# Optimization experiments

Measured on AMD Instinct MI355X. Metric: run time of the kernel, lower is better.

The kernel has to match this reference:

```python
import jax, jax.numpy as jnp
import numpy as np

N = 100000      # nodes
D_IN = 512      # in_size
D_OUT = 512     # out_size
E = 200000      # edges per etype
EPS = 1e-5      # LayerNorm eps


def setup_inputs() -> dict:
    key = jax.random.key(0)
    ks = jax.random.split(key, 10)
    scale = 1.0 / np.sqrt(D_IN)
    inp = {
        "x": jax.random.normal(ks[0], (N, D_IN), jnp.float32),
        "W0": jax.random.normal(ks[1], (D_OUT, D_IN), jnp.float32) * scale,
        "W1": jax.random.normal(ks[2], (D_OUT, D_IN), jnp.float32) * scale,
        "W2": jax.random.normal(ks[3], (D_OUT, D_IN), jnp.float32) * scale,
        "gamma": jnp.ones((D_OUT,), jnp.float32),
        "beta": jnp.zeros((D_OUT,), jnp.float32),
        "src0": jax.random.randint(ks[4], (E,), 0, N, jnp.int32),
        "dst0": jax.random.randint(ks[5], (E,), 0, N, jnp.int32),
        "src1": jax.random.randint(ks[6], (E,), 0, N, jnp.int32),
        "dst1": jax.random.randint(ks[7], (E,), 0, N, jnp.int32),
        "src2": jax.random.randint(ks[8], (E,), 0, N, jnp.int32),
        "dst2": jax.random.randint(ks[9], (E,), 0, N, jnp.int32),
    }
    return inp


def _segment_mean(msgs, dst, n):
    # per-dst-node mean; 0 for nodes with no incoming edges (DGL fn.mean semantics)
    s = jax.ops.segment_sum(msgs, dst, num_segments=n)
    c = jax.ops.segment_sum(jnp.ones((msgs.shape[0],), msgs.dtype), dst, num_segments=n)
    return s / jnp.maximum(c, 1.0)[:, None]


def reference(x, W0, W1, W2, gamma, beta, src0, dst0, src1, dst1, src2, dst2):
    # relation-specific linear transforms, averaged over etypes sharing the src ntype
    h = (x @ W0.T + x @ W1.T + x @ W2.T) / 3.0            # [N, D_OUT]
    # per-etype copy_u / mean aggregation
    a0 = _segment_mean(h[src0], dst0, N)
    a1 = _segment_mean(h[src1], dst1, N)
    a2 = _segment_mean(h[src2], dst2, N)
    # cross-etype 'mean' reducer
    h_agg = (a0 + a1 + a2) / 3.0
    # LayerNorm(ReLU(h_agg))
    a = jax.nn.relu(h_agg)
    mu = jnp.mean(a, axis=-1, keepdims=True)
    var = jnp.mean(jnp.square(a - mu), axis=-1, keepdims=True)
    return (a - mu) * jax.lax.rsqrt(var + EPS) * gamma + beta
```

## Files before the change

### kernel.cpp

```cpp
#include <hip/hip_runtime.h>
#include <cstdint>
#include <cstddef>

#define N_NODES 100000
#define DIM 512
#define NE 200000
#define NBLK 391

typedef __attribute__((ext_vector_type(4))) float floatx4;
typedef __attribute__((ext_vector_type(8))) short shortx8;

__device__ __forceinline__ unsigned short f2bf(float f) {
    union { float f; uint32_t u; } v; v.f = f;
    uint32_t r = v.u + 0x7fff + ((v.u >> 16) & 1);
    return (unsigned short)(r >> 16);
}

__device__ __forceinline__ float bf2f(unsigned short h) {
    union { uint32_t u; float f; } v; v.u = ((uint32_t)h) << 16;
    return v.f;
}

__device__ __forceinline__ void load_lds16(const void* g, void* l) {
    __builtin_amdgcn_global_load_lds(
        (const __attribute__((address_space(1))) uint32_t*)g,
        (__attribute__((address_space(3))) uint32_t*)l, 16, 0, 0);
}

__global__ __launch_bounds__(256) void combine_w_kernel(
    const float* __restrict__ W0, const float* __restrict__ W1,
    const float* __restrict__ W2, unsigned short* __restrict__ Wc) {
    int i = blockIdx.x * 256 + threadIdx.x;
    Wc[i] = f2bf((W0[i] + W1[i] + W2[i]) * (1.0f / 3.0f));
}

__global__ __launch_bounds__(256) void convert_x_kernel(
    const float* __restrict__ x, unsigned short* __restrict__ xb) {
    size_t t = (size_t)blockIdx.x * 256 + threadIdx.x;
    const float4* xp = (const float4*)(x + t * 8);
    float4 v0 = xp[0];
    float4 v1 = xp[1];
    ushort4 o0, o1;
    o0.x = f2bf(v0.x); o0.y = f2bf(v0.y); o0.z = f2bf(v0.z); o0.w = f2bf(v0.w);
    o1.x = f2bf(v1.x); o1.y = f2bf(v1.y); o1.z = f2bf(v1.z); o1.w = f2bf(v1.w);
    ushort4* op = (ushort4*)(xb + t * 8);
    op[0] = o0;
    op[1] = o1;
}

__global__ __launch_bounds__(256) void count_kernel(
    const int* __restrict__ d0, const int* __restrict__ d1,
    const int* __restrict__ d2, int* __restrict__ cnt) {
    int t = blockIdx.x * 256 + threadIdx.x;
    if (t >= 3 * NE) return;
    int e = t / NE;
    int i = t - e * NE;
    const int* dp = (e == 0) ? d0 : (e == 1) ? d1 : d2;
    atomicAdd(&cnt[e * N_NODES + dp[i]], 1);
}

__global__ __launch_bounds__(256) void scan1_kernel(
    const int* __restrict__ cnt, int* __restrict__ bsum) {
    int t = threadIdx.x;
    int n = blockIdx.x * 256 + t;
    int rl = 0;
    if (n < N_NODES) rl = cnt[n] + cnt[N_NODES + n] + cnt[2 * N_NODES + n];
    int v = rl;
    #pragma unroll
    for (int off = 32; off > 0; off >>= 1) v += __shfl_xor(v, off);
    __shared__ int ws_[4];
    if ((t & 63) == 0) ws_[t >> 6] = v;
    __syncthreads();
    if (t == 0) bsum[blockIdx.x] = ws_[0] + ws_[1] + ws_[2] + ws_[3];
}

__global__ __launch_bounds__(512) void scan2_kernel(
    const int* __restrict__ bsum, int* __restrict__ boff) {
    __shared__ int sh[512];
    int t = threadIdx.x;
    int v = (t < NBLK) ? bsum[t] : 0;
    sh[t] = v;
    __syncthreads();
    #pragma unroll
    for (int off = 1; off < 512; off <<= 1) {
        int add = (t >= off) ? sh[t - off] : 0;
        __syncthreads();
        sh[t] += add;
        __syncthreads();
    }
    if (t < NBLK) boff[t] = sh[t] - v;
}

__global__ __launch_bounds__(256) void scan3_kernel(
    const int* __restrict__ cnt, const int* __restrict__ boff,
    int* __restrict__ row_start, int* __restrict__ cursor) {
    __shared__ int sh[256];
    int t = threadIdx.x;
    int n = blockIdx.x * 256 + t;
    int rl = 0;
    if (n < N_NODES) rl = cnt[n] + cnt[N_NODES + n] + cnt[2 * N_NODES + n];
    sh[t] = rl;
    __syncthreads();
    #pragma unroll
    for (int off = 1; off < 256; off <<= 1) {
        int add = (t >= off) ? sh[t - off] : 0;
        __syncthreads();
        sh[t] += add;
        __syncthreads();
    }
    if (n < N_NODES) {
        int excl = sh[t] - rl + boff[blockIdx.x];
        row_start[n] = excl;
        cursor[n] = excl;
    }
}

__global__ __launch_bounds__(256) void bin_kernel(
    const int* __restrict__ s0, const int* __restrict__ d0,
    const int* __restrict__ s1, const int* __restrict__ d1,
    const int* __restrict__ s2, const int* __restrict__ d2,
    int* __restrict__ cursor, int* __restrict__ src_tag) {
    int t = blockIdx.x * 256 + threadIdx.x;
    if (t >= 3 * NE) return;
    int e = t / NE;
    int i = t - e * NE;
    const int* sp; const int* dp;
    if (e == 0)      { sp = s0; dp = d0; }
    else if (e == 1) { sp = s1; dp = d1; }
    else             { sp = s2; dp = d2; }
    int d = dp[i];
    int pos = atomicAdd(&cursor[d], 1);
    src_tag[pos] = sp[i] | (e << 30);
}

__global__ __launch_bounds__(256) void gemm_kernel(
    const unsigned short* __restrict__ A, const unsigned short* __restrict__ B,
    unsigned short* __restrict__ H, int M) {
    __shared__ alignas(16) unsigned short As[128 * 32];
    __shared__ alignas(16) unsigned short Bs[128 * 32];
    const int tid = threadIdx.x;
    const int lane = tid & 63;
    const int w = tid >> 6;
    const int wr = w >> 1, wc = w & 1;
    const int q = lane >> 4, r = lane & 15;

    int lid = ((int)blockIdx.x & 7) * 391 + ((int)blockIdx.x >> 3);
    int mt = lid >> 2, nt = lid & 3;
    int m0 = mt * 128, n0 = nt * 128;

    floatx4 acc[4][4] = {};

    for (int k0 = 0; k0 < DIM; k0 += 32) {
        #pragma unroll
        for (int i = 0; i < 2; ++i) {
            int ca = i * 256 + tid;
            int row = ca >> 2, c = ca & 3;
            int gm = m0 + row; if (gm >= M) gm = M - 1;
            load_lds16(&A[(size_t)gm * DIM + k0 + c * 8], &As[ca * 8]);
            load_lds16(&B[(size_t)(n0 + row) * DIM + k0 + c * 8], &Bs[ca * 8]);
        }
        __syncthreads();
        shortx8 af[4], bfr[4];
        #pragma unroll
        for (int mi = 0; mi < 4; ++mi)
            af[mi] = *(const shortx8*)&As[(wr * 64 + mi * 16 + r) * 32 + q * 8];
        #pragma unroll
        for (int nj = 0; nj < 4; ++nj)
            bfr[nj] = *(const shortx8*)&Bs[(wc * 64 + nj * 16 + r) * 32 + q * 8];
        #pragma unroll
        for (int mi = 0; mi < 4; ++mi)
            #pragma unroll
            for (int nj = 0; nj < 4; ++nj)
                acc[mi][nj] = __builtin_amdgcn_mfma_f32_16x16x32_bf16(
                    af[mi], bfr[nj], acc[mi][nj], 0, 0, 0);
        __syncthreads();
    }

    #pragma unroll
    for (int mi = 0; mi < 4; ++mi) {
        #pragma unroll
        for (int rg = 0; rg < 4; ++rg) {
            int gm = m0 + wr * 64 + mi * 16 + q * 4 + rg;
            if (gm < M) {
                #pragma unroll
                for (int nj = 0; nj < 4; ++nj)
                    H[(size_t)gm * DIM + n0 + wc * 64 + nj * 16 + r] =
                        f2bf(acc[mi][nj][rg]);
            }
        }
    }
}

__global__ __launch_bounds__(256) void gather_ln_kernel(
    const unsigned short* __restrict__ h, const int* __restrict__ row_start,
    const int* __restrict__ cnt, const int* __restrict__ src_tag,
    const float* __restrict__ gamma, const float* __restrict__ beta,
    float* __restrict__ out) {
    const int lane = threadIdx.x & 63;
    const int n = blockIdx.x * 4 + (threadIdx.x >> 6);
    if (n >= N_NODES) return;
    const int c0 = cnt[n], c1 = cnt[N_NODES + n], c2 = cnt[2 * N_NODES + n];
    const int len = c0 + c1 + c2;
    const float w0 = 1.0f / (3.0f * (float)max(c0, 1));
    const float w1 = 1.0f / (3.0f * (float)max(c1, 1));
    const float w2 = 1.0f / (3.0f * (float)max(c2, 1));
    const int beg = row_start[n];
    float acc[8] = {};
    for (int base = 0; base < len; base += 64) {
        int rem = len - base;
        int m = rem < 64 ? rem : 64;
        int tag = (lane < m) ? src_tag[beg + base + lane] : 0;
        for (int j = 0; j < m; ++j) {
            int u = __shfl(tag, j);
            int e = ((unsigned)u) >> 30;
            int s = u & 0x3FFFFFFF;
            float wgt = (e == 0) ? w0 : ((e == 1) ? w1 : w2);
            shortx8 v = *(const shortx8*)(h + (size_t)s * DIM + lane * 8);
            #pragma unroll
            for (int k = 0; k < 8; ++k)
                acc[k] += bf2f((unsigned short)v[k]) * wgt;
        }
    }
    float s1_ = 0.0f, s2_ = 0.0f;
    #pragma unroll
    for (int k = 0; k < 8; ++k) {
        float v = fmaxf(acc[k], 0.0f);
        acc[k] = v; s1_ += v; s2_ += v * v;
    }
    #pragma unroll
    for (int off = 1; off < 64; off <<= 1) {
        s1_ += __shfl_xor(s1_, off);
        s2_ += __shfl_xor(s2_, off);
    }
    float mu = s1_ * (1.0f / DIM);
    float var = s2_ * (1.0f / DIM) - mu * mu;
    float rstd = rsqrtf(var + 1e-5f);
    float4 g0 = *(const float4*)(gamma + lane * 8);
    float4 g1 = *(const float4*)(gamma + lane * 8 + 4);
    float4 b0 = *(const float4*)(beta + lane * 8);
    float4 b1 = *(const float4*)(beta + lane * 8 + 4);
    float4 o0, o1;
    o0.x = (acc[0] - mu) * rstd * g0.x + b0.x;
    o0.y = (acc[1] - mu) * rstd * g0.y + b0.y;
    o0.z = (acc[2] - mu) * rstd * g0.z + b0.z;
    o0.w = (acc[3] - mu) * rstd * g0.w + b0.w;
    o1.x = (acc[4] - mu) * rstd * g1.x + b1.x;
    o1.y = (acc[5] - mu) * rstd * g1.y + b1.y;
    o1.z = (acc[6] - mu) * rstd * g1.z + b1.z;
    o1.w = (acc[7] - mu) * rstd * g1.w + b1.w;
    float4* op = (float4*)(out + (size_t)n * DIM + lane * 8);
    op[0] = o0;
    op[1] = o1;
}

extern "C" void kernel_launch(void* const* d_in, const int* in_sizes, int n_in,
                              void* d_out, int out_size, void* d_ws, size_t ws_size,
                              hipStream_t stream) {
    const float* x     = (const float*)d_in[0];
    const float* W0    = (const float*)d_in[1];
    const float* W1    = (const float*)d_in[2];
    const float* W2    = (const float*)d_in[3];
    const float* gamma = (const float*)d_in[4];
    const float* beta  = (const float*)d_in[5];
    const int* s0  = (const int*)d_in[6];
    const int* dd0 = (const int*)d_in[7];
    const int* s1  = (const int*)d_in[8];
    const int* dd1 = (const int*)d_in[9];
    const int* s2  = (const int*)d_in[10];
    const int* dd2 = (const int*)d_in[11];
    float* out = (float*)d_out;

    char* ws = (char*)d_ws;
    size_t off = 0;
    int* cnt = (int*)(ws + off);             off += 3u * N_NODES * 4u;
    int* row_start = (int*)(ws + off);       off += (size_t)N_NODES * 4u;
    int* cursor = (int*)(ws + off);          off += (size_t)N_NODES * 4u;
    int* bsum = (int*)(ws + off);            off += 2048;
    int* boff = (int*)(ws + off);            off += 2048;
    int* src_tag = (int*)(ws + off);         off += (size_t)3 * NE * 4u;
    unsigned short* Wc = (unsigned short*)(ws + off); off += (size_t)DIM * DIM * 2u;
    off = (off + 255) & ~255ull;
    unsigned short* xb = (unsigned short*)(ws + off); off += (size_t)N_NODES * DIM * 2u;
    off = (off + 255) & ~255ull;
    unsigned short* h = (unsigned short*)(ws + off);

    hipMemsetAsync(cnt, 0, (size_t)3 * N_NODES * sizeof(int), stream);

    combine_w_kernel<<<(DIM * DIM) / 256, 256, 0, stream>>>(W0, W1, W2, Wc);
    convert_x_kernel<<<(N_NODES * DIM / 8) / 256, 256, 0, stream>>>(x, xb);
    count_kernel<<<(3 * NE + 255) / 256, 256, 0, stream>>>(dd0, dd1, dd2, cnt);
    scan1_kernel<<<NBLK, 256, 0, stream>>>(cnt, bsum);
    scan2_kernel<<<1, 512, 0, stream>>>(bsum, boff);
    scan3_kernel<<<NBLK, 256, 0, stream>>>(cnt, boff, row_start, cursor);
    bin_kernel<<<(3 * NE + 255) / 256, 256, 0, stream>>>(
        s0, dd0, s1, dd1, s2, dd2, cursor, src_tag);

    gemm_kernel<<<3128, 256, 0, stream>>>(xb, Wc, h, N_NODES);

    gather_ln_kernel<<<(N_NODES + 3) / 4, 256, 0, stream>>>(
        h, row_start, cnt, src_tag, gamma, beta, out);
}
```

Measured before the change: 620.7 us.

## Fuse fp32-to-bf16 conversion of x into GEMM and unroll gather loop

Removes the separate convert_x kernel: the GEMM now loads fp32 rows of x into registers, converts them to bf16 and writes them to LDS itself, prefetching the next k-slice while the MFMAs run. This drops one full write and re-read of a bf16 copy of x. In exchange, each GEMM block reads fp32 A data (twice the bytes) once per N-tile, four times in total, and does the conversion inline. Separately, the gather loop is unrolled by four so several row loads are in flight at once.

```diff
diff --git a/kernel.cpp b/kernel.cpp
--- a/kernel.cpp
+++ b/kernel.cpp
@@ -32,20 +32,6 @@
     const float* __restrict__ W2, unsigned short* __restrict__ Wc) {
     int i = blockIdx.x * 256 + threadIdx.x;
     Wc[i] = f2bf((W0[i] + W1[i] + W2[i]) * (1.0f / 3.0f));
-}
-
-__global__ __launch_bounds__(256) void convert_x_kernel(
-    const float* __restrict__ x, unsigned short* __restrict__ xb) {
-    size_t t = (size_t)blockIdx.x * 256 + threadIdx.x;
-    const float4* xp = (const float4*)(x + t * 8);
-    float4 v0 = xp[0];
-    float4 v1 = xp[1];
-    ushort4 o0, o1;
-    o0.x = f2bf(v0.x); o0.y = f2bf(v0.y); o0.z = f2bf(v0.z); o0.w = f2bf(v0.w);
-    o1.x = f2bf(v1.x); o1.y = f2bf(v1.y); o1.z = f2bf(v1.z); o1.w = f2bf(v1.w);
-    ushort4* op = (ushort4*)(xb + t * 8);
-    op[0] = o0;
-    op[1] = o1;
 }
 
 __global__ __launch_bounds__(256) void count_kernel(
@@ -134,7 +120,7 @@
 }
 
 __global__ __launch_bounds__(256) void gemm_kernel(
-    const unsigned short* __restrict__ A, const unsigned short* __restrict__ B,
+    const float* __restrict__ X, const unsigned short* __restrict__ B,
     unsigned short* __restrict__ H, int M) {
     __shared__ alignas(16) unsigned short As[128 * 32];
     __shared__ alignas(16) unsigned short Bs[128 * 32];
@@ -148,18 +134,40 @@
     int mt = lid >> 2, nt = lid & 3;
     int m0 = mt * 128, n0 = nt * 128;
 
+    int arow0 = tid >> 2, ac8 = tid & 3;
+    int gm0 = m0 + arow0;       if (gm0 >= M) gm0 = M - 1;
+    int gm1 = m0 + arow0 + 64;  if (gm1 >= M) gm1 = M - 1;
+    const float* ap0 = X + (size_t)gm0 * DIM + ac8 * 8;
+    const float* ap1 = X + (size_t)gm1 * DIM + ac8 * 8;
+
+    float4 a00, a01, a10, a11;
+    #define ALOAD(k0_) do { \
+        a00 = *(const float4*)(ap0 + (k0_));     a01 = *(const float4*)(ap0 + (k0_) + 4); \
+        a10 = *(const float4*)(ap1 + (k0_));     a11 = *(const float4*)(ap1 + (k0_) + 4); \
+    } while (0)
+
     floatx4 acc[4][4] = {};
+    ALOAD(0);
 
     for (int k0 = 0; k0 < DIM; k0 += 32) {
         #pragma unroll
         for (int i = 0; i < 2; ++i) {
-            int ca = i * 256 + tid;
-            int row = ca >> 2, c = ca & 3;
-            int gm = m0 + row; if (gm >= M) gm = M - 1;
-            load_lds16(&A[(size_t)gm * DIM + k0 + c * 8], &As[ca * 8]);
-            load_lds16(&B[(size_t)(n0 + row) * DIM + k0 + c * 8], &Bs[ca * 8]);
-        }
-        __syncthreads();
+            int cb = i * 256 + tid;
+            int row = cb >> 2, c = cb & 3;
+            load_lds16(&B[(size_t)(n0 + row) * DIM + k0 + c * 8], &Bs[cb * 8]);
+        }
+        {
+            shortx8 p0, p1;
+            p0[0] = f2bf(a00.x); p0[1] = f2bf(a00.y); p0[2] = f2bf(a00.z); p0[3] = f2bf(a00.w);
+            p0[4] = f2bf(a01.x); p0[5] = f2bf(a01.y); p0[6] = f2bf(a01.z); p0[7] = f2bf(a01.w);
+            p1[0] = f2bf(a10.x); p1[1] = f2bf(a10.y); p1[2] = f2bf(a10.z); p1[3] = f2bf(a10.w);
+            p1[4] = f2bf(a11.x); p1[5] = f2bf(a11.y); p1[6] = f2bf(a11.z); p1[7] = f2bf(a11.w);
+            *(shortx8*)&As[tid * 8] = p0;
+            *(shortx8*)&As[(tid + 256) * 8] = p1;
+        }
+        __syncthreads();
+        if (k0 + 32 < DIM) ALOAD(k0 + 32);
+
         shortx8 af[4], bfr[4];
         #pragma unroll
         for (int mi = 0; mi < 4; ++mi)
@@ -175,6 +183,7 @@
                     af[mi], bfr[nj], acc[mi][nj], 0, 0, 0);
         __syncthreads();
     }
+    #undef ALOAD
 
     #pragma unroll
     for (int mi = 0; mi < 4; ++mi) {
@@ -205,20 +214,42 @@
     const float w1 = 1.0f / (3.0f * (float)max(c1, 1));
     const float w2 = 1.0f / (3.0f * (float)max(c2, 1));
     const int beg = row_start[n];
+    const size_t lx = (size_t)lane * 8;
     float acc[8] = {};
     for (int base = 0; base < len; base += 64) {
         int rem = len - base;
         int m = rem < 64 ? rem : 64;
         int tag = (lane < m) ? src_tag[beg + base + lane] : 0;
-        for (int j = 0; j < m; ++j) {
+        int j = 0;
+        for (; j + 4 <= m; j += 4) {
+            int u0 = __shfl(tag, j),     u1 = __shfl(tag, j + 1);
+            int u2 = __shfl(tag, j + 2), u3 = __shfl(tag, j + 3);
+            int e0 = ((unsigned)u0) >> 30, e1 = ((unsigned)u1) >> 30;
+            int e2 = ((unsigned)u2) >> 30, e3 = ((unsigned)u3) >> 30;
+            float g0 = (e0 == 0) ? w0 : ((e0 == 1) ? w1 : w2);
+            float g1 = (e1 == 0) ? w0 : ((e1 == 1) ? w1 : w2);
+            float g2 = (e2 == 0) ? w0 : ((e2 == 1) ? w1 : w2);
+            float g3 = (e3 == 0) ? w0 : ((e3 == 1) ? w1 : w2);
+            shortx8 v0 = *(const shortx8*)(h + (size_t)(u0 & 0x3FFFFFFF) * DIM + lx);
+            shortx8 v1 = *(const shortx8*)(h + (size_t)(u1 & 0x3FFFFFFF) * DIM + lx);
+            shortx8 v2 = *(const shortx8*)(h + (size_t)(u2 & 0x3FFFFFFF) * DIM + lx);
+            shortx8 v3 = *(const shortx8*)(h + (size_t)(u3 & 0x3FFFFFFF) * DIM + lx);
+            #pragma unroll
+            for (int k = 0; k < 8; ++k) {
+                acc[k] += bf2f((unsigned short)v0[k]) * g0;
+                acc[k] += bf2f((unsigned short)v1[k]) * g1;
+                acc[k] += bf2f((unsigned short)v2[k]) * g2;
+                acc[k] += bf2f((unsigned short)v3[k]) * g3;
+            }
+        }
+        for (; j < m; ++j) {
             int u = __shfl(tag, j);
             int e = ((unsigned)u) >> 30;
-            int s = u & 0x3FFFFFFF;
-            float wgt = (e == 0) ? w0 : ((e == 1) ? w1 : w2);
-            shortx8 v = *(const shortx8*)(h + (size_t)s * DIM + lane * 8);
+            float wg = (e == 0) ? w0 : ((e == 1) ? w1 : w2);
+            shortx8 v = *(const shortx8*)(h + (size_t)(u & 0x3FFFFFFF) * DIM + lx);
             #pragma unroll
             for (int k = 0; k < 8; ++k)
-                acc[k] += bf2f((unsigned short)v[k]) * wgt;
+                acc[k] += bf2f((unsigned short)v[k]) * wg;
         }
     }
     float s1_ = 0.0f, s2_ = 0.0f;
@@ -280,14 +311,11 @@
     int* src_tag = (int*)(ws + off);         off += (size_t)3 * NE * 4u;
     unsigned short* Wc = (unsigned short*)(ws + off); off += (size_t)DIM * DIM * 2u;
     off = (off + 255) & ~255ull;
-    unsigned short* xb = (unsigned short*)(ws + off); off += (size_t)N_NODES * DIM * 2u;
-    off = (off + 255) & ~255ull;
     unsigned short* h = (unsigned short*)(ws + off);
 
     hipMemsetAsync(cnt, 0, (size_t)3 * N_NODES * sizeof(int), stream);
 
     combine_w_kernel<<<(DIM * DIM) / 256, 256, 0, stream>>>(W0, W1, W2, Wc);
-    convert_x_kernel<<<(N_NODES * DIM / 8) / 256, 256, 0, stream>>>(x, xb);
     count_kernel<<<(3 * NE + 255) / 256, 256, 0, stream>>>(dd0, dd1, dd2, cnt);
     scan1_kernel<<<NBLK, 256, 0, stream>>>(cnt, bsum);
     scan2_kernel<<<1, 512, 0, stream>>>(bsum, boff);
@@ -295,7 +323,7 @@
     bin_kernel<<<(3 * NE + 255) / 256, 256, 0, stream>>>(
         s0, dd0, s1, dd1, s2, dd2, cursor, src_tag);
 
-    gemm_kernel<<<3128, 256, 0, stream>>>(xb, Wc, h, N_NODES);
+    gemm_kernel<<<3128, 256, 0, stream>>>(x, Wc, h, N_NODES);
 
     gather_ln_kernel<<<(N_NODES + 3) / 4, 256, 0, stream>>>(
         h, row_start, cnt, src_tag, gamma, beta, out);
```

Result: faster. 575.7 us (-7.3%).
